# Kernel optimization log

Measured on AMD Instinct MI355X. Metric: run time of the kernel, lower is better.

## Reference

```python
import jax, jax.numpy as jnp
import numpy as np

N_NODES = 500_000
N_EDGES = 16_000_000
F_IN, F_HID, F_OUT = 5, 5, 8


def _gcn_conv(x, W, b, src, dst, norm, n):
    # x: [N, Fin] -> transform first (cheaper than transforming messages)
    h = x @ W                              # [N, Fout]
    msg = h[src] * norm[:, None]           # [E', Fout] gather + per-edge scale
    out = jax.ops.segment_sum(msg, dst, num_segments=n)  # scatter-add over dst
    return out + b


def setup_inputs() -> dict:
    key = jax.random.key(0)
    ks = jax.random.split(key, 6)
    x = jax.random.normal(ks[0], (N_NODES, F_IN), dtype=jnp.float32)
    edge_index = jax.random.randint(ks[1], (2, N_EDGES), 0, N_NODES, dtype=jnp.int32)
    # Glorot-ish init for the two GCNConv layers
    W1 = jax.random.normal(ks[2], (F_IN, F_HID), dtype=jnp.float32) / np.sqrt(F_IN)
    b1 = jnp.zeros((F_HID,), dtype=jnp.float32)
    W2 = jax.random.normal(ks[3], (F_HID, F_OUT), dtype=jnp.float32) / np.sqrt(F_HID)
    b2 = jnp.zeros((F_OUT,), dtype=jnp.float32)
    return {"x": x, "edge_index": edge_index, "W1": W1, "b1": b1, "W2": W2, "b2": b2}


def reference(x, edge_index, W1, b1, W2, b2):
    n = x.shape[0]
    # GCNConv default: add self-loops, symmetric D^-1/2 A D^-1/2 normalization
    loops = jnp.arange(n, dtype=edge_index.dtype)
    src = jnp.concatenate([edge_index[0], loops])
    dst = jnp.concatenate([edge_index[1], loops])
    deg = jax.ops.segment_sum(jnp.ones_like(dst, dtype=x.dtype), dst, num_segments=n)
    dinv = jnp.where(deg > 0, jax.lax.rsqrt(deg), 0.0)
    norm = dinv[src] * dinv[dst]           # [E + N]

    h = _gcn_conv(x, W1, b1, src, dst, norm, n)
    h = jax.nn.relu(h)
    # F.dropout with training=False is the identity (eval-mode reference)
    h = _gcn_conv(h, W2, b2, src, dst, norm, n)
    return jax.nn.log_softmax(h, axis=1)
```

## Files before the change

### kernel.cpp

```cpp
#include <hip/hip_runtime.h>
#include <math.h>


#define FIN 5
#define FHID 5
#define FOUT 8
#define RB 256
#define EPA 32768
#define NBUCK_MAX 2048
#define OCAP 10240

typedef _Float16 half8 __attribute__((ext_vector_type(8)));
typedef int int4v __attribute__((ext_vector_type(4)));
typedef float fl4 __attribute__((ext_vector_type(4)));


__global__ void k_scan1(const int* __restrict__ t, int* __restrict__ scn,
                        int* __restrict__ partial, int n) {
    __shared__ int sh[256];
    int tx = threadIdx.x;
    int i = blockIdx.x * 256 + tx;
    int v = (i < n) ? t[i] : 0;
    sh[tx] = v;
    __syncthreads();
    for (int off = 1; off < 256; off <<= 1) {
        int add = (tx >= off) ? sh[tx - off] : 0;
        __syncthreads();
        sh[tx] += add;
        __syncthreads();
    }
    if (i < n) scn[i] = sh[tx] - v;
    if (tx == 255) partial[blockIdx.x] = sh[255];
}

__global__ void k_scan2(int* __restrict__ partial, int nb) {
    __shared__ int sh[256];
    __shared__ int carry;
    int tx = threadIdx.x;
    if (tx == 0) carry = 0;
    __syncthreads();
    for (int base = 0; base < nb; base += 256) {
        int i = base + tx;
        int v = (i < nb) ? partial[i] : 0;
        int c0 = carry;
        sh[tx] = v;
        __syncthreads();
        for (int off = 1; off < 256; off <<= 1) {
            int add = (tx >= off) ? sh[tx - off] : 0;
            __syncthreads();
            sh[tx] += add;
            __syncthreads();
        }
        if (i < nb) partial[i] = c0 + sh[tx] - v;
        __syncthreads();
        if (tx == 0) carry = c0 + sh[255];
        __syncthreads();
    }
}


__global__ void k_histA(const int* __restrict__ dst, int* __restrict__ cnt,
                        int e, int nbuck, int nblkA) {
    __shared__ int hist[NBUCK_MAX];
    int tx = threadIdx.x, blk = blockIdx.x;
    for (int b = tx; b < nbuck; b += 1024) hist[b] = 0;
    __syncthreads();
    size_t base = (size_t)blk * EPA;
    const int4v* dst4 = (const int4v*)dst;
    for (int k = 0; k < EPA / 4096; ++k) {
        size_t e4 = base / 4 + (size_t)k * 1024 + tx;
        size_t i = e4 * 4;
        if (i + 3 < (size_t)e) {
            int4v d4 = __builtin_nontemporal_load(&dst4[e4]);
#pragma unroll
            for (int j = 0; j < 4; ++j) atomicAdd(&hist[d4[j] >> 8], 1);
        } else {
            for (int j = 0; j < 4; ++j) {
                size_t ii = i + j;
                if (ii < (size_t)e) atomicAdd(&hist[dst[ii] >> 8], 1);
            }
        }
    }
    __syncthreads();
    for (int b = tx; b < nbuck; b += 1024) cnt[(size_t)b * nblkA + blk] = hist[b];
}

__global__ void k_scatterA(const int* __restrict__ src, const int* __restrict__ dst,
                           const int* __restrict__ cnt,
                           const int* __restrict__ scn, const int* __restrict__ part,
                           unsigned int* __restrict__ binnedA,
                           int e, int nbuck, int nblkA) {
    __shared__ int lstart[NBUCK_MAX];
    __shared__ int cur[NBUCK_MAX];
    __shared__ int gbase[NBUCK_MAX];
    __shared__ unsigned int staged[EPA];
    int tx = threadIdx.x, blk = blockIdx.x;
    for (int b = tx; b < NBUCK_MAX; b += 1024) {
        if (b < nbuck) {
            size_t idx = (size_t)b * nblkA + blk;
            lstart[b] = cnt[idx];
            gbase[b] = scn[idx] + part[idx >> 8];
        } else {
            lstart[b] = 0;
        }
    }
    __syncthreads();
    int j0 = tx, j1 = tx + 1024;
    int c0 = lstart[j0], c1 = lstart[j1];
    for (int off = 1; off < NBUCK_MAX; off <<= 1) {
        int a0 = (j0 >= off) ? lstart[j0 - off] : 0;
        int a1 = (j1 >= off) ? lstart[j1 - off] : 0;
        __syncthreads();
        lstart[j0] += a0; lstart[j1] += a1;
        __syncthreads();
    }
    int e0 = lstart[j0] - c0, e1 = lstart[j1] - c1;
    __syncthreads();
    lstart[j0] = e0; lstart[j1] = e1;
    cur[j0] = e0;    cur[j1] = e1;
    __syncthreads();
    size_t base = (size_t)blk * EPA;
    const int4v* dst4 = (const int4v*)dst;
    const int4v* src4 = (const int4v*)src;
    for (int k = 0; k < EPA / 4096; ++k) {
        size_t e4 = base / 4 + (size_t)k * 1024 + tx;
        size_t i = e4 * 4;
        if (i + 3 < (size_t)e) {
            int4v d4 = __builtin_nontemporal_load(&dst4[e4]);
            int4v s4 = __builtin_nontemporal_load(&src4[e4]);
#pragma unroll
            for (int j = 0; j < 4; ++j) {
                int d = d4[j];
                int pos = atomicAdd(&cur[d >> 8], 1);
                staged[pos] = ((unsigned int)(d & (RB - 1)) << 19) | (unsigned int)s4[j];
            }
        } else {
            for (int j = 0; j < 4; ++j) {
                size_t ii = i + j;
                if (ii < (size_t)e) {
                    int d = dst[ii];
                    int pos = atomicAdd(&cur[d >> 8], 1);
                    staged[pos] = ((unsigned int)(d & (RB - 1)) << 19) | (unsigned int)src[ii];
                }
            }
        }
    }
    __syncthreads();
    int grp = tx >> 4, lane = tx & 15;
    for (int b = grp; b < nbuck; b += 64) {
        int ls = lstart[b];
        int le = (b + 1 < NBUCK_MAX) ? lstart[b + 1] : 0;
        int len = le - ls;
        int gb = gbase[b];
        for (int k = lane; k < len; k += 16)
            binnedA[gb + k] = staged[ls + k];
    }
}


__global__ void k_passC(const unsigned int* __restrict__ binnedA,
                        const int* __restrict__ scn, const int* __restrict__ part,
                        const float* __restrict__ x,
                        half8* __restrict__ g1, unsigned int* __restrict__ binned3,
                        int* __restrict__ p0ptr, int* __restrict__ p1ptr,
                        int n, int e, int nbuck, int nblkA, unsigned int half) {
    __shared__ int hist[2 * RB];
    __shared__ int scanbuf[2 * RB];
    __shared__ int cur[2 * RB];
    __shared__ unsigned int obuf[OCAP];
    int tx = threadIdx.x, b = blockIdx.x;
    hist[tx] = 0;
    __syncthreads();
    size_t i0 = (size_t)b * nblkA;
    int start = scn[i0] + part[i0 >> 8];
    int end;
    if (b + 1 < nbuck) {
        size_t i1 = (size_t)(b + 1) * nblkA;
        end = scn[i1] + part[i1 >> 8];
    } else {
        end = e;
    }
    int len = end - start;
    bool stage = (len <= OCAP);
    unsigned int r[20];
    if (stage) {
#pragma unroll
        for (int k = 0; k < 20; ++k) {
            int i = start + k * 512 + tx;
            if (i < end) {
                unsigned int p = binnedA[i];
                r[k] = p;
                int key = ((p & 0x7FFFFu) >= half ? 256 : 0) | (int)(p >> 19);
                atomicAdd(&hist[key], 1);
            }
        }
    } else {
        for (int i = start + tx; i < end; i += 512) {
            unsigned int p = binnedA[i];
            int key = ((p & 0x7FFFFu) >= half ? 256 : 0) | (int)(p >> 19);
            atomicAdd(&hist[key], 1);
        }
    }
    __syncthreads();
    int v = hist[tx];
    scanbuf[tx] = v;
    __syncthreads();
    for (int off = 1; off < 2 * RB; off <<= 1) {
        int add = (tx >= off) ? scanbuf[tx - off] : 0;
        __syncthreads();
        scanbuf[tx] += add;
        __syncthreads();
    }
    int excl = scanbuf[tx] - v;
    cur[tx] = excl;
    if (tx < 256) p0ptr[(size_t)b * RB + tx] = start + excl;
    else          p1ptr[(size_t)b * RB + (tx - 256)] = start + excl;
    if (tx < RB) {
        int node = b * RB + tx;
        if (node < n) {
            int deg = hist[tx] + hist[256 + tx];
            float d = rsqrtf((float)(deg + 1));
            const float* xp = x + (size_t)node * FIN;
            half8 row = {};
#pragma unroll
            for (int f = 0; f < FIN; ++f) row[f] = (_Float16)(xp[f] * d);
            row[5] = (_Float16)d;
            g1[node] = row;
        }
    }
    if (b == nbuck - 1 && tx == 0) p0ptr[(size_t)nbuck * RB] = end;
    __syncthreads();
    if (stage) {
#pragma unroll
        for (int k = 0; k < 20; ++k) {
            int i = start + k * 512 + tx;
            if (i < end) {
                unsigned int p = r[k];
                int key = ((p & 0x7FFFFu) >= half ? 256 : 0) | (int)(p >> 19);
                int pos = atomicAdd(&cur[key], 1);
                obuf[pos] = p & 0x7FFFFu;
            }
        }
        __syncthreads();
        for (int j = tx; j < len; j += 512)
            binned3[start + j] = obuf[j];
    } else {
        for (int i = start + tx; i < end; i += 512) {
            unsigned int p = binnedA[i];
            int key = ((p & 0x7FFFFu) >= half ? 256 : 0) | (int)(p >> 19);
            int pos = atomicAdd(&cur[key], 1);
            binned3[start + pos] = p & 0x7FFFFu;
        }
    }
}


__global__ void k_vphase0(const unsigned int* __restrict__ ed,
                          const int* __restrict__ p0, const int* __restrict__ p1,
                          const half8* __restrict__ g,
                          fl4* __restrict__ acc4, float* __restrict__ acc1, int n) {
    int tid = blockIdx.x * blockDim.x + threadIdx.x;
    int node = tid >> 4;
    int lane = tid & 15;
    if (node >= n) return;
    int dl = node & (RB - 1);
    int o0 = p0[node];
    int oe = (dl == RB - 1) ? p1[node & ~(RB - 1)] : p0[node + 1];
    float a0 = 0, a1 = 0, a2 = 0, a3 = 0, a4 = 0;
    for (int k = o0 + lane; k < oe; k += 16) {
        unsigned int s = __builtin_nontemporal_load(&ed[k]);
        half8 hv = g[s];
        a0 += (float)hv[0]; a1 += (float)hv[1]; a2 += (float)hv[2];
        a3 += (float)hv[3]; a4 += (float)hv[4];
    }
#pragma unroll
    for (int off = 1; off < 16; off <<= 1) {
        a0 += __shfl_xor(a0, off, 16);
        a1 += __shfl_xor(a1, off, 16);
        a2 += __shfl_xor(a2, off, 16);
        a3 += __shfl_xor(a3, off, 16);
        a4 += __shfl_xor(a4, off, 16);
    }
    if (lane == 0) {
        fl4 p; p.x = a0; p.y = a1; p.z = a2; p.w = a3;
        __builtin_nontemporal_store(p, &acc4[node]);
        __builtin_nontemporal_store(a4, &acc1[node]);
    }
}

__global__ void k_vp1_l1(const unsigned int* __restrict__ ed,
                         const int* __restrict__ p0, const int* __restrict__ p1,
                         const half8* __restrict__ g1,
                         const fl4* __restrict__ acc4, const float* __restrict__ acc1,
                         const float* __restrict__ W1, const float* __restrict__ b1,
                         half8* __restrict__ g2, int n) {
    int tid = blockIdx.x * blockDim.x + threadIdx.x;
    int node = tid >> 4;
    int lane = tid & 15;
    if (node >= n) return;
    int dl = node & (RB - 1);
    int o0 = p1[node];
    int oe = (dl == RB - 1) ? p0[(node & ~(RB - 1)) + RB] : p1[node + 1];
    float a0 = 0, a1 = 0, a2 = 0, a3 = 0, a4 = 0;
    for (int k = o0 + lane; k < oe; k += 16) {
        unsigned int s = __builtin_nontemporal_load(&ed[k]);
        half8 hv = g1[s];
        a0 += (float)hv[0]; a1 += (float)hv[1]; a2 += (float)hv[2];
        a3 += (float)hv[3]; a4 += (float)hv[4];
    }
#pragma unroll
    for (int off = 1; off < 16; off <<= 1) {
        a0 += __shfl_xor(a0, off, 16);
        a1 += __shfl_xor(a1, off, 16);
        a2 += __shfl_xor(a2, off, 16);
        a3 += __shfl_xor(a3, off, 16);
        a4 += __shfl_xor(a4, off, 16);
    }
    if (lane == 0) {
        fl4 pp = acc4[node];
        float p4 = acc1[node];
        half8 gi = g1[node];
        float d = (float)gi[5];
        float v[FIN];
        v[0] = (a0 + pp.x + (float)gi[0]) * d;
        v[1] = (a1 + pp.y + (float)gi[1]) * d;
        v[2] = (a2 + pp.z + (float)gi[2]) * d;
        v[3] = (a3 + pp.w + (float)gi[3]) * d;
        v[4] = (a4 + p4   + (float)gi[4]) * d;
        half8 go = {};
#pragma unroll
        for (int j = 0; j < FHID; ++j) {
            float s = b1[j];
#pragma unroll
            for (int k = 0; k < FIN; ++k) s = fmaf(v[k], W1[k * FHID + j], s);
            go[j] = (_Float16)(fmaxf(s, 0.0f) * d);
        }
        go[5] = gi[5];
        g2[node] = go;
    }
}

__global__ void k_vp1_l2(const unsigned int* __restrict__ ed,
                         const int* __restrict__ p0, const int* __restrict__ p1,
                         const half8* __restrict__ g2,
                         const fl4* __restrict__ acc4, const float* __restrict__ acc1,
                         const float* __restrict__ W2, const float* __restrict__ b2,
                         float* __restrict__ out, int n) {
    int tid = blockIdx.x * blockDim.x + threadIdx.x;
    int node = tid >> 4;
    int lane = tid & 15;
    if (node >= n) return;
    int dl = node & (RB - 1);
    int o0 = p1[node];
    int oe = (dl == RB - 1) ? p0[(node & ~(RB - 1)) + RB] : p1[node + 1];
    float a0 = 0, a1 = 0, a2 = 0, a3 = 0, a4 = 0;
    for (int k = o0 + lane; k < oe; k += 16) {
        unsigned int s = __builtin_nontemporal_load(&ed[k]);
        half8 hv = g2[s];
        a0 += (float)hv[0]; a1 += (float)hv[1]; a2 += (float)hv[2];
        a3 += (float)hv[3]; a4 += (float)hv[4];
    }
#pragma unroll
    for (int off = 1; off < 16; off <<= 1) {
        a0 += __shfl_xor(a0, off, 16);
        a1 += __shfl_xor(a1, off, 16);
        a2 += __shfl_xor(a2, off, 16);
        a3 += __shfl_xor(a3, off, 16);
        a4 += __shfl_xor(a4, off, 16);
    }
    fl4 pp = acc4[node];
    float p4 = acc1[node];
    half8 gi = g2[node];
    float d = (float)gi[5];
    float v[FHID];
    v[0] = (a0 + pp.x + (float)gi[0]) * d;
    v[1] = (a1 + pp.y + (float)gi[1]) * d;
    v[2] = (a2 + pp.z + (float)gi[2]) * d;
    v[3] = (a3 + pp.w + (float)gi[3]) * d;
    v[4] = (a4 + p4   + (float)gi[4]) * d;
    int j = lane & 7;
    float oj = b2[j];
#pragma unroll
    for (int k = 0; k < FHID; ++k) oj = fmaf(v[k], W2[k * FOUT + j], oj);
    float mx = oj;
#pragma unroll
    for (int off = 1; off < 8; off <<= 1) mx = fmaxf(mx, __shfl_xor(mx, off, 8));
    float ex = expf(oj - mx);
    float ss = ex;
#pragma unroll
    for (int off = 1; off < 8; off <<= 1) ss += __shfl_xor(ss, off, 8);
    if (lane < 8) out[(size_t)node * FOUT + j] = oj - mx - logf(ss);
}


__global__ void f_init_deg(float* __restrict__ deg, int n) {
    int i = blockIdx.x * blockDim.x + threadIdx.x;
    if (i < n) deg[i] = 1.0f;
}
__global__ void f_count_deg(const int* __restrict__ dst, float* __restrict__ deg, int e) {
    int i = blockIdx.x * blockDim.x + threadIdx.x;
    if (i < e) atomicAdd(&deg[dst[i]], 1.0f);
}
__global__ void f_finish_deg_g1(const float* __restrict__ x, float* __restrict__ dinv,
                                float* __restrict__ g1, int n) {
    int i = blockIdx.x * blockDim.x + threadIdx.x;
    if (i >= n) return;
    float d = rsqrtf(dinv[i]);
    dinv[i] = d;
#pragma unroll
    for (int f = 0; f < FIN; ++f) g1[(size_t)i * FIN + f] = x[(size_t)i * FIN + f] * d;
}
__global__ void f_scatter5(const int* __restrict__ src, const int* __restrict__ dst,
                           const float* __restrict__ g, float* __restrict__ acc, int e) {
    int i = blockIdx.x * blockDim.x + threadIdx.x;
    if (i >= e) return;
    int s = src[i], d = dst[i];
    float* a = acc + (size_t)d * 5;
    const float* gp = g + (size_t)s * 5;
    atomicAdd(a + 0, gp[0]);
    atomicAdd(a + 1, gp[1]);
    atomicAdd(a + 2, gp[2]);
    atomicAdd(a + 3, gp[3]);
    atomicAdd(a + 4, gp[4]);
}
__global__ void f_update1(const float* __restrict__ dinv, float* __restrict__ g,
                          float* __restrict__ acc, const float* __restrict__ W1,
                          const float* __restrict__ b1, int n) {
    int i = blockIdx.x * blockDim.x + threadIdx.x;
    if (i >= n) return;
    float d = dinv[i];
    float v[FIN];
#pragma unroll
    for (int f = 0; f < FIN; ++f) {
        size_t idx = (size_t)i * FIN + f;
        v[f] = (acc[idx] + g[idx]) * d;
        acc[idx] = 0.0f;
    }
#pragma unroll
    for (int j = 0; j < FHID; ++j) {
        float s = b1[j];
#pragma unroll
        for (int k = 0; k < FIN; ++k) s += v[k] * W1[k * FHID + j];
        g[(size_t)i * FHID + j] = fmaxf(s, 0.0f) * d;
    }
}
__global__ void f_update2(const float* __restrict__ dinv, const float* __restrict__ g,
                          const float* __restrict__ acc, const float* __restrict__ W2,
                          const float* __restrict__ b2, float* __restrict__ out, int n) {
    int i = blockIdx.x * blockDim.x + threadIdx.x;
    if (i >= n) return;
    float d = dinv[i];
    float v[FHID];
#pragma unroll
    for (int f = 0; f < FHID; ++f) v[f] = (acc[(size_t)i * FHID + f] + g[(size_t)i * FHID + f]) * d;
    float o[FOUT];
    float m = -1e30f;
#pragma unroll
    for (int j = 0; j < FOUT; ++j) {
        float s = b2[j];
#pragma unroll
        for (int k = 0; k < FHID; ++k) s += v[k] * W2[k * FOUT + j];
        o[j] = s;
        m = fmaxf(m, s);
    }
    float ssum = 0.0f;
#pragma unroll
    for (int j = 0; j < FOUT; ++j) ssum += expf(o[j] - m);
    float lse = m + logf(ssum);
#pragma unroll
    for (int j = 0; j < FOUT; ++j) out[(size_t)i * FOUT + j] = o[j] - lse;
}


extern "C" void kernel_launch(void* const* d_in, const int* in_sizes, int n_in,
                              void* d_out, int out_size, void* d_ws, size_t ws_size,
                              hipStream_t stream) {
    const float* x  = (const float*)d_in[0];
    const int*   ei = (const int*)d_in[1];
    const float* W1 = (const float*)d_in[2];
    const float* b1 = (const float*)d_in[3];
    const float* W2 = (const float*)d_in[4];
    const float* b2 = (const float*)d_in[5];

    const int n = in_sizes[0] / FIN;
    const int e = in_sizes[1] / 2;
    const int* src = ei;
    const int* dst = ei + e;

    const int nbuck = (n + RB - 1) / RB;
    const int nblkA = (e + EPA - 1) / EPA;
    const size_t m = (size_t)nbuck * nblkA;
    const int nsb = (int)((m + 255) / 256);

    size_t off = 0;
    auto al = [&](size_t bytes) { size_t o = off; off = (off + bytes + 15) & ~(size_t)15; return o; };
    int*          cnt     = (int*)((char*)d_ws + al(m * 4));
    int*          scn     = (int*)((char*)d_ws + al(m * 4));
    int*          part    = (int*)((char*)d_ws + al((size_t)nsb * 4));
    int*          p0ptr   = (int*)((char*)d_ws + al(((size_t)nbuck * RB + 1) * 4));
    int*          p1ptr   = (int*)((char*)d_ws + al((size_t)nbuck * RB * 4));
    half8*        g1      = (half8*)((char*)d_ws + al((size_t)n * 16));
    unsigned int* binnedA = (unsigned int*)((char*)d_ws + al((size_t)e * 4));
    unsigned int* binned3 = (unsigned int*)((char*)d_ws + al((size_t)e * 4));
    half8*        g2      = (half8*)binnedA;
    fl4*          acc4    = (fl4*)((char*)binnedA + (size_t)16 * 1024 * 1024);
    float*        acc1    = (float*)((char*)binnedA + (size_t)32 * 1024 * 1024);
    const size_t need = off;

    if (ws_size >= need && n <= 524288 && n >= 1 && (e & 3) == 0 && nbuck <= NBUCK_MAX &&
        (size_t)e * 4 >= (size_t)34 * 1024 * 1024 && (size_t)n * 16 <= (size_t)16 * 1024 * 1024) {
        const unsigned int half = (unsigned int)(n >> 1);
        k_histA<<<nblkA, 1024, 0, stream>>>(dst, cnt, e, nbuck, nblkA);
        k_scan1<<<nsb, 256, 0, stream>>>(cnt, scn, part, (int)m);
        k_scan2<<<1, 256, 0, stream>>>(part, nsb);
        k_scatterA<<<nblkA, 1024, 0, stream>>>(src, dst, cnt, scn, part, binnedA, e, nbuck, nblkA);
        k_passC<<<nbuck, 512, 0, stream>>>(binnedA, scn, part, x, g1, binned3, p0ptr, p1ptr,
                                           n, e, nbuck, nblkA, half);
        const int ga = (int)(((size_t)n * 16 + 511) / 512);
        k_vphase0<<<ga, 512, 0, stream>>>(binned3, p0ptr, p1ptr, g1, acc4, acc1, n);
        k_vp1_l1<<<ga, 512, 0, stream>>>(binned3, p0ptr, p1ptr, g1, acc4, acc1, W1, b1, g2, n);
        k_vphase0<<<ga, 512, 0, stream>>>(binned3, p0ptr, p1ptr, g2, acc4, acc1, n);
        k_vp1_l2<<<ga, 512, 0, stream>>>(binned3, p0ptr, p1ptr, g2, acc4, acc1, W2, b2, (float*)d_out, n);
        return;
    }

    const int B = 256;
    const int gn = (n + B - 1) / B;
    const int ge = (e + B - 1) / B;
    float* fdinv = (float*)d_ws;
    float* fg    = fdinv + n;
    float* facc  = fg + (size_t)5 * n;
    hipMemsetAsync(facc, 0, (size_t)5 * n * sizeof(float), stream);
    f_init_deg<<<gn, B, 0, stream>>>(fdinv, n);
    f_count_deg<<<ge, B, 0, stream>>>(dst, fdinv, e);
    f_finish_deg_g1<<<gn, B, 0, stream>>>(x, fdinv, fg, n);
    f_scatter5<<<ge, B, 0, stream>>>(src, dst, fg, facc, e);
    f_update1<<<gn, B, 0, stream>>>(fdinv, fg, facc, W1, b1, n);
    f_scatter5<<<ge, B, 0, stream>>>(src, dst, fg, facc, e);
    f_update2<<<gn, B, 0, stream>>>(fdinv, fg, facc, W2, b2, (float*)d_out, n);
}
```

Baseline: 452.1 us.

## Fuse two-phase half-split neighbor gathers into single kernel per layer

Replaces the separate phase-0 gather kernel and the phase-1 gather-plus-update kernel with one kernel per layer. In it, lanes 0-7 walk the first source-half edge range and lanes 8-15 walk the second, then a shuffle reduction combines them. This removes two launches and the intermediate acc4/acc1 writes and reads. In exchange, both halves of the feature table are gathered at once, which may reduce the cache locality the half-split was designed to provide. The workspace guard is relaxed to match.

```diff
diff --git a/kernel.cpp b/kernel.cpp
--- a/kernel.cpp
+++ b/kernel.cpp
@@ -255,21 +255,34 @@
 }
 
 
-__global__ void k_vphase0(const unsigned int* __restrict__ ed,
-                          const int* __restrict__ p0, const int* __restrict__ p1,
-                          const half8* __restrict__ g,
-                          fl4* __restrict__ acc4, float* __restrict__ acc1, int n) {
+__device__ __forceinline__ void fused_ranges(const int* __restrict__ p0,
+                                             const int* __restrict__ p1,
+                                             int node, int lane, int& st, int& en) {
+    int dl = node & (RB - 1);
+    int q0  = p0[node];
+    int q0e = (dl == RB - 1) ? p1[node & ~(RB - 1)] : p0[node + 1];
+    int q1  = p1[node];
+    int q1e = (dl == RB - 1) ? p0[(node & ~(RB - 1)) + RB] : p1[node + 1];
+    bool ph0 = (lane < 8);
+    st = (ph0 ? q0 : q1) + (lane & 7);
+    en = ph0 ? q0e : q1e;
+}
+
+__global__ void k_fused1(const unsigned int* __restrict__ ed,
+                         const int* __restrict__ p0, const int* __restrict__ p1,
+                         const half8* __restrict__ g1,
+                         const float* __restrict__ W1, const float* __restrict__ b1,
+                         half8* __restrict__ g2, int n) {
     int tid = blockIdx.x * blockDim.x + threadIdx.x;
     int node = tid >> 4;
     int lane = tid & 15;
     if (node >= n) return;
-    int dl = node & (RB - 1);
-    int o0 = p0[node];
-    int oe = (dl == RB - 1) ? p1[node & ~(RB - 1)] : p0[node + 1];
+    int st, en;
+    fused_ranges(p0, p1, node, lane, st, en);
     float a0 = 0, a1 = 0, a2 = 0, a3 = 0, a4 = 0;
-    for (int k = o0 + lane; k < oe; k += 16) {
+    for (int k = st; k < en; k += 8) {
         unsigned int s = __builtin_nontemporal_load(&ed[k]);
-        half8 hv = g[s];
+        half8 hv = g1[s];
         a0 += (float)hv[0]; a1 += (float)hv[1]; a2 += (float)hv[2];
         a3 += (float)hv[3]; a4 += (float)hv[4];
     }
@@ -282,29 +295,42 @@
         a4 += __shfl_xor(a4, off, 16);
     }
     if (lane == 0) {
-        fl4 p; p.x = a0; p.y = a1; p.z = a2; p.w = a3;
-        __builtin_nontemporal_store(p, &acc4[node]);
-        __builtin_nontemporal_store(a4, &acc1[node]);
-    }
-}
-
-__global__ void k_vp1_l1(const unsigned int* __restrict__ ed,
+        half8 gi = g1[node];
+        float d = (float)gi[5];
+        float v[FIN];
+        v[0] = (a0 + (float)gi[0]) * d;
+        v[1] = (a1 + (float)gi[1]) * d;
+        v[2] = (a2 + (float)gi[2]) * d;
+        v[3] = (a3 + (float)gi[3]) * d;
+        v[4] = (a4 + (float)gi[4]) * d;
+        half8 go = {};
+#pragma unroll
+        for (int j = 0; j < FHID; ++j) {
+            float s = b1[j];
+#pragma unroll
+            for (int k = 0; k < FIN; ++k) s = fmaf(v[k], W1[k * FHID + j], s);
+            go[j] = (_Float16)(fmaxf(s, 0.0f) * d);
+        }
+        go[5] = gi[5];
+        g2[node] = go;
+    }
+}
+
+__global__ void k_fused2(const unsigned int* __restrict__ ed,
                          const int* __restrict__ p0, const int* __restrict__ p1,
-                         const half8* __restrict__ g1,
-                         const fl4* __restrict__ acc4, const float* __restrict__ acc1,
-                         const float* __restrict__ W1, const float* __restrict__ b1,
-                         half8* __restrict__ g2, int n) {
+                         const half8* __restrict__ g2,
+                         const float* __restrict__ W2, const float* __restrict__ b2,
+                         float* __restrict__ out, int n) {
     int tid = blockIdx.x * blockDim.x + threadIdx.x;
     int node = tid >> 4;
     int lane = tid & 15;
     if (node >= n) return;
-    int dl = node & (RB - 1);
-    int o0 = p1[node];
-    int oe = (dl == RB - 1) ? p0[(node & ~(RB - 1)) + RB] : p1[node + 1];
+    int st, en;
+    fused_ranges(p0, p1, node, lane, st, en);
     float a0 = 0, a1 = 0, a2 = 0, a3 = 0, a4 = 0;
-    for (int k = o0 + lane; k < oe; k += 16) {
+    for (int k = st; k < en; k += 8) {
         unsigned int s = __builtin_nontemporal_load(&ed[k]);
-        half8 hv = g1[s];
+        half8 hv = g2[s];
         a0 += (float)hv[0]; a1 += (float)hv[1]; a2 += (float)hv[2];
         a3 += (float)hv[3]; a4 += (float)hv[4];
     }
@@ -316,68 +342,14 @@
         a3 += __shfl_xor(a3, off, 16);
         a4 += __shfl_xor(a4, off, 16);
     }
-    if (lane == 0) {
-        fl4 pp = acc4[node];
-        float p4 = acc1[node];
-        half8 gi = g1[node];
-        float d = (float)gi[5];
-        float v[FIN];
-        v[0] = (a0 + pp.x + (float)gi[0]) * d;
-        v[1] = (a1 + pp.y + (float)gi[1]) * d;
-        v[2] = (a2 + pp.z + (float)gi[2]) * d;
-        v[3] = (a3 + pp.w + (float)gi[3]) * d;
-        v[4] = (a4 + p4   + (float)gi[4]) * d;
-        half8 go = {};
-#pragma unroll
-        for (int j = 0; j < FHID; ++j) {
-            float s = b1[j];
-#pragma unroll
-            for (int k = 0; k < FIN; ++k) s = fmaf(v[k], W1[k * FHID + j], s);
-            go[j] = (_Float16)(fmaxf(s, 0.0f) * d);
-        }
-        go[5] = gi[5];
-        g2[node] = go;
-    }
-}
-
-__global__ void k_vp1_l2(const unsigned int* __restrict__ ed,
-                         const int* __restrict__ p0, const int* __restrict__ p1,
-                         const half8* __restrict__ g2,
-                         const fl4* __restrict__ acc4, const float* __restrict__ acc1,
-                         const float* __restrict__ W2, const float* __restrict__ b2,
-                         float* __restrict__ out, int n) {
-    int tid = blockIdx.x * blockDim.x + threadIdx.x;
-    int node = tid >> 4;
-    int lane = tid & 15;
-    if (node >= n) return;
-    int dl = node & (RB - 1);
-    int o0 = p1[node];
-    int oe = (dl == RB - 1) ? p0[(node & ~(RB - 1)) + RB] : p1[node + 1];
-    float a0 = 0, a1 = 0, a2 = 0, a3 = 0, a4 = 0;
-    for (int k = o0 + lane; k < oe; k += 16) {
-        unsigned int s = __builtin_nontemporal_load(&ed[k]);
-        half8 hv = g2[s];
-        a0 += (float)hv[0]; a1 += (float)hv[1]; a2 += (float)hv[2];
-        a3 += (float)hv[3]; a4 += (float)hv[4];
-    }
-#pragma unroll
-    for (int off = 1; off < 16; off <<= 1) {
-        a0 += __shfl_xor(a0, off, 16);
-        a1 += __shfl_xor(a1, off, 16);
-        a2 += __shfl_xor(a2, off, 16);
-        a3 += __shfl_xor(a3, off, 16);
-        a4 += __shfl_xor(a4, off, 16);
-    }
-    fl4 pp = acc4[node];
-    float p4 = acc1[node];
     half8 gi = g2[node];
     float d = (float)gi[5];
     float v[FHID];
-    v[0] = (a0 + pp.x + (float)gi[0]) * d;
-    v[1] = (a1 + pp.y + (float)gi[1]) * d;
-    v[2] = (a2 + pp.z + (float)gi[2]) * d;
-    v[3] = (a3 + pp.w + (float)gi[3]) * d;
-    v[4] = (a4 + p4   + (float)gi[4]) * d;
+    v[0] = (a0 + (float)gi[0]) * d;
+    v[1] = (a1 + (float)gi[1]) * d;
+    v[2] = (a2 + (float)gi[2]) * d;
+    v[3] = (a3 + (float)gi[3]) * d;
+    v[4] = (a4 + (float)gi[4]) * d;
     int j = lane & 7;
     float oj = b2[j];
 #pragma unroll
@@ -503,12 +475,10 @@
     unsigned int* binnedA = (unsigned int*)((char*)d_ws + al((size_t)e * 4));
     unsigned int* binned3 = (unsigned int*)((char*)d_ws + al((size_t)e * 4));
     half8*        g2      = (half8*)binnedA;
-    fl4*          acc4    = (fl4*)((char*)binnedA + (size_t)16 * 1024 * 1024);
-    float*        acc1    = (float*)((char*)binnedA + (size_t)32 * 1024 * 1024);
     const size_t need = off;
 
     if (ws_size >= need && n <= 524288 && n >= 1 && (e & 3) == 0 && nbuck <= NBUCK_MAX &&
-        (size_t)e * 4 >= (size_t)34 * 1024 * 1024 && (size_t)n * 16 <= (size_t)16 * 1024 * 1024) {
+        (size_t)e * 4 >= (size_t)n * 16) {
         const unsigned int half = (unsigned int)(n >> 1);
         k_histA<<<nblkA, 1024, 0, stream>>>(dst, cnt, e, nbuck, nblkA);
         k_scan1<<<nsb, 256, 0, stream>>>(cnt, scn, part, (int)m);
@@ -517,10 +487,8 @@
         k_passC<<<nbuck, 512, 0, stream>>>(binnedA, scn, part, x, g1, binned3, p0ptr, p1ptr,
                                            n, e, nbuck, nblkA, half);
         const int ga = (int)(((size_t)n * 16 + 511) / 512);
-        k_vphase0<<<ga, 512, 0, stream>>>(binned3, p0ptr, p1ptr, g1, acc4, acc1, n);
-        k_vp1_l1<<<ga, 512, 0, stream>>>(binned3, p0ptr, p1ptr, g1, acc4, acc1, W1, b1, g2, n);
-        k_vphase0<<<ga, 512, 0, stream>>>(binned3, p0ptr, p1ptr, g2, acc4, acc1, n);
-        k_vp1_l2<<<ga, 512, 0, stream>>>(binned3, p0ptr, p1ptr, g2, acc4, acc1, W2, b2, (float*)d_out, n);
+        k_fused1<<<ga, 512, 0, stream>>>(binned3, p0ptr, p1ptr, g1, W1, b1, g2, n);
+        k_fused2<<<ga, 512, 0, stream>>>(binned3, p0ptr, p1ptr, g2, W2, b2, (float*)d_out, n);
         return;
     }
 
```

New measurement: 491.1 us. +8.6%, slower.
